# Kernel tuning notes

Hardware: AMD Instinct MI355X
Metric: run time of the kernel (lower is better)

## Reference

```python
import jax, jax.numpy as jnp
import numpy as np

D_MODEL, D_STATE, N_HEADS = 1024, 64, 16


def setup_inputs() -> dict:
    key = jax.random.key(0)
    ks = jax.random.split(key, 4)
    B, T = 4, 4096
    s = 1.0 / np.sqrt(D_MODEL)
    x = jax.random.normal(ks[0], (B, T, D_MODEL), dtype=jnp.float32)
    h_prev = jnp.zeros((B, N_HEADS, D_STATE), dtype=jnp.float32)
    gate_w = jax.random.normal(ks[1], (2 * N_HEADS * D_STATE, D_MODEL), dtype=jnp.float32) * s
    # torch init: forget-gate bias = 1, input-gate bias = 0
    gate_b = jnp.concatenate([jnp.ones(N_HEADS * D_STATE), jnp.zeros(N_HEADS * D_STATE)]).astype(jnp.float32)
    value_w = jax.random.normal(ks[2], (N_HEADS * D_STATE, D_MODEL), dtype=jnp.float32) * s
    out_w = jax.random.normal(ks[3], (D_MODEL, N_HEADS * D_STATE), dtype=jnp.float32) * s
    return {"x": x, "h_prev": h_prev, "gate_w": gate_w, "gate_b": gate_b, "value_w": value_w, "out_w": out_w}


def reference(x, h_prev, gate_w, gate_b, value_w, out_w):
    B, T, _ = x.shape
    H, S = N_HEADS, D_STATE
    gates = (jnp.einsum('btd,gd->btg', x, gate_w) + gate_b).reshape(B, T, 2, H, S)
    A = jax.nn.sigmoid(gates[:, :, 0])   # [B,T,H,S] forget gate
    Bg = jax.nn.sigmoid(gates[:, :, 1])  # [B,T,H,S] input gate
    V = jnp.einsum('btd,vd->btv', x, value_w).reshape(B, T, H, S)

    def step(h, inp):
        a_t, bv_t = inp
        h = a_t * h + bv_t
        return h, h

    # time-major for scan; precompute B*V elementwise product
    a_tm = jnp.moveaxis(A, 1, 0)                # [T,B,H,S]
    bv_tm = jnp.moveaxis(Bg * V, 1, 0)          # [T,B,H,S]
    h_last, h_seq = jax.lax.scan(step, h_prev, (a_tm, bv_tm))
    h_flat = jnp.moveaxis(h_seq, 0, 1).reshape(B, T, H * S)
    y = jnp.einsum('btv,dv->btd', h_flat, out_w)  # dropout is identity at p=0/eval
    return y, h_last
```

## Files before the change

kernel.cpp:

```cpp
#include <hip/hip_runtime.h>
#include <cstdint>
#include <cstddef>


typedef _Float16 f16;
typedef _Float16 f16x2 __attribute__((ext_vector_type(2)));
typedef _Float16 f16x8 __attribute__((ext_vector_type(8)));
typedef float    f32x4 __attribute__((ext_vector_type(4)));

__device__ __forceinline__ void gload_lds16(const void* g, void* l) {
  __builtin_amdgcn_global_load_lds(
      (const __attribute__((address_space(1))) void*)g,
      (__attribute__((address_space(3))) void*)l, 16, 0, 0);
}

__device__ __forceinline__ float sigmoidf_(float x) {
  return 1.0f / (1.0f + __expf(-x));
}

__global__ __launch_bounds__(256) void cast_pack(
    const float* __restrict__ x, const float* __restrict__ gw,
    const float* __restrict__ vw, const float* __restrict__ ow,
    f16* __restrict__ xh, f16* __restrict__ wgv, f16* __restrict__ owb) {
  const int XG = 2097152, GG = 262144, VG = 131072, OG = 131072;
  int id = blockIdx.x * 256 + threadIdx.x;
  const float* src;
  f16* dst;
  if (id < XG) {
    src = x + (size_t)id * 8;
    dst = xh + (size_t)id * 8;
  } else if (id < XG + GG) {
    int g = id - XG;
    int row = g >> 7, col = g & 127;
    int drow = (row < 1024) ? row : (1024 + 2 * (row - 1024));
    src = gw + ((size_t)row << 10) + col * 8;
    dst = wgv + ((size_t)drow << 10) + col * 8;
  } else if (id < XG + GG + VG) {
    int g = id - XG - GG;
    int row = g >> 7, col = g & 127;
    int drow = 1024 + 2 * row + 1;
    src = vw + ((size_t)row << 10) + col * 8;
    dst = wgv + ((size_t)drow << 10) + col * 8;
  } else if (id < XG + GG + VG + OG) {
    int g = id - XG - GG - VG;
    src = ow + (size_t)g * 8;
    dst = owb + (size_t)g * 8;
  } else {
    return;
  }
  float4 v0 = ((const float4*)src)[0], v1 = ((const float4*)src)[1];
  f16x8 o;
  o[0] = (f16)v0.x; o[1] = (f16)v0.y; o[2] = (f16)v0.z; o[3] = (f16)v0.w;
  o[4] = (f16)v1.x; o[5] = (f16)v1.y; o[6] = (f16)v1.z; o[7] = (f16)v1.w;
  *(f16x8*)dst = o;
}

template <int EPI>
__global__ __launch_bounds__(512, 2) void gemm256(
    const f16* __restrict__ A, const f16* __restrict__ Bw,
    const float* __restrict__ gate_b, void* __restrict__ o0v,
    void* __restrict__ o1v, int Mtiles) {
  constexpr int K = 1024;
  __shared__ __align__(16) f16 SH[65536];
  f16* LA = SH;
  f16* LB = SH + 32768;

  const int tid  = threadIdx.x;
  const int lane = tid & 63;
  const int l15  = lane & 15;
  const int oct4 = lane >> 4;
  const int wid  = tid >> 6;
  const int wr   = wid >> 2;
  const int wc   = wid & 3;

  const int nwg = gridDim.x;
  const int bid = blockIdx.x;
  const int swz = (bid & 7) * (nwg >> 3) + (bid >> 3);
  const int m0 = (swz % Mtiles) * 256;
  const int n0 = (swz / Mtiles) * 256;

  const int srow = tid >> 2;
  const int soct = (tid & 3) ^ ((srow >> 1) & 3);
  const f16* Ag = A  + (size_t)(n0 + srow) * K + soct * 8;
  const f16* Bg = Bw + (size_t)(m0 + srow) * K + soct * 8;
  f16* Al = LA + tid * 8;
  f16* Bl = LB + tid * 8;

  const int fswz  = oct4 ^ ((l15 >> 1) & 3);
  const int aslot = (wr * 128 + l15) * 4 + fswz;
  const int bslot = (wc * 64 + l15) * 4 + fswz;

  f32x4 acc[8][4];
#pragma unroll
  for (int mm = 0; mm < 8; ++mm)
#pragma unroll
    for (int nn = 0; nn < 4; ++nn)
#pragma unroll
      for (int e = 0; e < 4; ++e) acc[mm][nn][e] = 0.f;

#define STAGE_A(tl, kh)                                          \
  do {                                                           \
    const f16* s_ = Ag + (tl) * 64 + (kh) * 32;                  \
    f16* d_ = Al + ((tl) & 1) * 16384 + (kh) * 8192;             \
    gload_lds16(s_, d_);                                         \
    gload_lds16(s_ + 128 * K, d_ + 4096);                        \
  } while (0)
#define STAGE_B(tl, kh)                                          \
  do {                                                           \
    const f16* s_ = Bg + (tl) * 64 + (kh) * 32;                  \
    f16* d_ = Bl + ((tl) & 1) * 16384 + (kh) * 8192;             \
    gload_lds16(s_, d_);                                         \
    gload_lds16(s_ + 128 * K, d_ + 4096);                        \
  } while (0)

  STAGE_A(0, 0); STAGE_B(0, 0);
  STAGE_A(0, 1); STAGE_B(0, 1);
  STAGE_A(1, 0); STAGE_B(1, 0);
  asm volatile("s_waitcnt vmcnt(8)" ::: "memory");
  __builtin_amdgcn_s_barrier();
  asm volatile("" ::: "memory");

  f16x8 bf[4];
  for (int i = 0; i < 8; ++i) {
    const bool last = (i == 7);
#pragma unroll
    for (int ph = 0; ph < 8; ++ph) {
      const int bb = ph >> 2;
      const int ks = (ph >> 1) & 1;
      const int h  = ph & 1;

      f16x8 af[4];
      if (h == 0) {
#pragma unroll
        for (int nn = 0; nn < 4; ++nn)
          bf[nn] = *(const f16x8*)&LB[bb * 16384 + ks * 8192 +
                                      (bslot + nn * 64) * 8];
      }
#pragma unroll
      for (int mm = 0; mm < 4; ++mm)
        af[mm] = *(const f16x8*)&LA[bb * 16384 + ks * 8192 +
                                    (aslot + (h * 4 + mm) * 64) * 8];

      {
        constexpr int toff[8] = {1, 1, 2, 2, 2, 2, 3, 3};
        constexpr int khv[8]  = {1, 1, 0, 0, 1, 1, 0, 0};
        if (!last || ph < 2) {
          const int tl = 2 * i + toff[ph];
          if (ph & 1) STAGE_B(tl, khv[ph]); else STAGE_A(tl, khv[ph]);
        }
      }

      __builtin_amdgcn_s_barrier();
      asm volatile("s_waitcnt lgkmcnt(0)" ::: "memory");

      __builtin_amdgcn_s_setprio(1);
#pragma unroll
      for (int mm = 0; mm < 4; ++mm)
#pragma unroll
        for (int nn = 0; nn < 4; ++nn)
          acc[h * 4 + mm][nn] = __builtin_amdgcn_mfma_f32_16x16x32_f16(
              af[mm], bf[nn], acc[h * 4 + mm][nn], 0, 0, 0);
      __builtin_amdgcn_s_setprio(0);

      if (ph & 1) {
        if (!last) {
          asm volatile("s_waitcnt vmcnt(8)" ::: "memory");
        } else if (ph == 1) {
          asm volatile("s_waitcnt vmcnt(8)" ::: "memory");
        } else if (ph == 3) {
          asm volatile("s_waitcnt vmcnt(4)" ::: "memory");
        } else if (ph == 5) {
          asm volatile("s_waitcnt vmcnt(0)" ::: "memory");
        }
      }
      __builtin_amdgcn_s_barrier();
      asm volatile("" ::: "memory");
    }
  }
#undef STAGE_A
#undef STAGE_B

  if (EPI == 1) {
    float* out = (float*)o0v;
#pragma unroll
    for (int mm = 0; mm < 8; ++mm)
#pragma unroll
      for (int nn = 0; nn < 4; ++nn) {
        const int m = m0 + wc * 64 + nn * 16 + l15;
#pragma unroll
        for (int r = 0; r < 4; ++r) {
          const int n = n0 + wr * 128 + mm * 16 + oct4 * 4 + r;
          out[(size_t)n * 1024 + m] = acc[mm][nn][r];
        }
      }
    return;
  }

  if (m0 < 1024) {
    float bias[4];
#pragma unroll
    for (int nn = 0; nn < 4; ++nn)
      bias[nn] = gate_b[m0 + wc * 64 + nn * 16 + l15];
    f16* o0 = (f16*)o0v;
#pragma unroll
    for (int ck = 0; ck < 2; ++ck) {
      __builtin_amdgcn_s_barrier();
      asm volatile("" ::: "memory");
      if (wr == ck) {
#pragma unroll
        for (int mm = 0; mm < 8; ++mm)
#pragma unroll
          for (int nn = 0; nn < 4; ++nn) {
            const int ch = wc * 64 + nn * 16 + l15;
#pragma unroll
            for (int r = 0; r < 4; ++r) {
              const int nl = mm * 16 + oct4 * 4 + r;
              SH[nl * 264 + ch] = (f16)sigmoidf_(acc[mm][nn][r] + bias[nn]);
            }
          }
      }
      __builtin_amdgcn_s_barrier();
      asm volatile("" ::: "memory");
#pragma unroll
      for (int j = 0; j < 8; ++j) {
        int s = j * 512 + tid;
        int row = s >> 5, sl = s & 31;
        f16x8 vv = *(const f16x8*)&SH[row * 264 + sl * 8];
        *(f16x8*)(o0 + (size_t)(n0 + ck * 128 + row) * 1024 + m0 + sl * 8) =
            vv;
      }
    }
  } else {
    const int c0 = (m0 - 1024) >> 1;
    float biasv[4];
#pragma unroll
    for (int nn = 0; nn < 4; ++nn) {
      const int ml = wc * 64 + nn * 16 + l15;
      biasv[nn] = gate_b[1024 + c0 + (ml >> 1)];
    }
    f16* o1 = (f16*)o1v;
#pragma unroll
    for (int ck = 0; ck < 2; ++ck) {
      __builtin_amdgcn_s_barrier();
      asm volatile("" ::: "memory");
      if (wr == ck) {
#pragma unroll
        for (int mm = 0; mm < 8; ++mm)
#pragma unroll
          for (int nn = 0; nn < 4; ++nn) {
            const int ml = wc * 64 + nn * 16 + l15;
#pragma unroll
            for (int r = 0; r < 4; ++r) {
              float val = acc[mm][nn][r];
              float pv = __shfl_xor(val, 1, 64);
              if (!(lane & 1)) {
                const int nl = mm * 16 + oct4 * 4 + r;
                SH[nl * 136 + (ml >> 1)] =
                    (f16)(sigmoidf_(val + biasv[nn]) * pv);
              }
            }
          }
      }
      __builtin_amdgcn_s_barrier();
      asm volatile("" ::: "memory");
#pragma unroll
      for (int j = 0; j < 4; ++j) {
        int s = j * 512 + tid;
        int row = s >> 4, sl = s & 15;
        f16x8 vv = *(const f16x8*)&SH[row * 136 + sl * 8];
        *(f16x8*)(o1 + (size_t)(n0 + ck * 128 + row) * 1024 + c0 + sl * 8) =
            vv;
      }
    }
  }
}

__global__ __launch_bounds__(256) void scan_pass1(
    const f16x2* __restrict__ a, const f16x2* __restrict__ bv,
    float2* __restrict__ Ac, float2* __restrict__ Uc) {
  const int c2 = blockIdx.x * 256 + threadIdx.x;
  const int j = blockIdx.y;
  const int b = blockIdx.z;
  const size_t base = ((size_t)(b * 4096 + j * 32)) * 512 + c2;
  float P0 = 1.f, P1 = 1.f, U0 = 0.f, U1 = 0.f;
#pragma unroll 8
  for (int t = 0; t < 32; ++t) {
    const size_t o = base + (size_t)t * 512;
    f16x2 at = a[o], bt = bv[o];
    float a0 = (float)at[0], a1 = (float)at[1];
    P0 *= a0; P1 *= a1;
    U0 = a0 * U0 + (float)bt[0];
    U1 = a1 * U1 + (float)bt[1];
  }
  const size_t o = ((size_t)(b * 128 + j)) * 512 + c2;
  Ac[o] = make_float2(P0, P1);
  Uc[o] = make_float2(U0, U1);
}

__global__ __launch_bounds__(256) void scan_pass2(
    const float* __restrict__ Ac, const float* __restrict__ Uc,
    const float* __restrict__ h_prev, float* __restrict__ Hs,
    float* __restrict__ hlast) {
  __shared__ float SA[4][64], SU[4][64];
  const int tid = threadIdx.x;
  const int seg = tid >> 6;
  const int cl  = tid & 63;
  const int ch  = blockIdx.x * 64 + cl;
  const int b = ch >> 10, c = ch & 1023;
  float A = 1.f, U = 0.f;
  for (int t = 0; t < 32; ++t) {
    const int j = seg * 32 + t;
    const size_t o = ((size_t)(b * 128 + j)) * 1024 + c;
    float av = Ac[o], uv = Uc[o];
    U = av * U + uv;
    A = av * A;
  }
  SA[seg][cl] = A;
  SU[seg][cl] = U;
  __syncthreads();
  float Ae = 1.f, Ue = 0.f;
  for (int s = 0; s < seg; ++s) {
    float av = SA[s][cl], uv = SU[s][cl];
    Ue = av * Ue + uv;
    Ae = av * Ae;
  }
  float H = Ae * h_prev[b * 1024 + c] + Ue;
  for (int t = 0; t < 32; ++t) {
    const int j = seg * 32 + t;
    const size_t o = ((size_t)(b * 128 + j)) * 1024 + c;
    Hs[o] = H;
    H = Ac[o] * H + Uc[o];
  }
  if (seg == 3) hlast[b * 1024 + c] = H;
}

__global__ __launch_bounds__(256) void scan_pass3(
    const f16x2* __restrict__ a, const f16x2* __restrict__ bv,
    const float2* __restrict__ Hs, f16x2* __restrict__ hb) {
  const int c2 = blockIdx.x * 256 + threadIdx.x;
  const int j = blockIdx.y;
  const int b = blockIdx.z;
  const size_t base = ((size_t)(b * 4096 + j * 32)) * 512 + c2;
  float2 H = Hs[((size_t)(b * 128 + j)) * 512 + c2];
  float h0 = H.x, h1 = H.y;
#pragma unroll 8
  for (int t = 0; t < 32; ++t) {
    const size_t o = base + (size_t)t * 512;
    f16x2 at = a[o], bt = bv[o];
    h0 = (float)at[0] * h0 + (float)bt[0];
    h1 = (float)at[1] * h1 + (float)bt[1];
    f16x2 hv; hv[0] = (f16)h0; hv[1] = (f16)h1;
    hb[o] = hv;
  }
}

extern "C" void kernel_launch(void* const* d_in, const int* in_sizes, int n_in,
                              void* d_out, int out_size, void* d_ws,
                              size_t ws_size, hipStream_t stream) {
  const float* x       = (const float*)d_in[0];
  const float* h_prev  = (const float*)d_in[1];
  const float* gate_w  = (const float*)d_in[2];
  const float* gate_b  = (const float*)d_in[3];
  const float* value_w = (const float*)d_in[4];
  const float* out_w   = (const float*)d_in[5];
  float* out = (float*)d_out;

  char* ws = (char*)d_ws;
  f16*   xh   = (f16*)(ws);
  f16*   wgv  = (f16*)(ws + 33554432);
  f16*   owb  = (f16*)(ws + 39845888);
  f16*   abuf = (f16*)(ws + 41943040);
  f16*   bvb  = (f16*)(ws + 75497472);
  float* Ac   = (float*)(ws + 109051904);
  float* Uc   = (float*)(ws + 111149056);
  float* Hs   = (float*)(ws + 113246208);
  float* hlast = out + 16777216;

  cast_pack<<<10240, 256, 0, stream>>>(x, gate_w, value_w, out_w, xh, wgv,
                                       owb);

  gemm256<0><<<dim3(768), 512, 0, stream>>>(xh, wgv, gate_b, abuf, bvb, 12);

  scan_pass1<<<dim3(2, 128, 4), 256, 0, stream>>>(
      (const f16x2*)abuf, (const f16x2*)bvb, (float2*)Ac, (float2*)Uc);
  scan_pass2<<<64, 256, 0, stream>>>(Ac, Uc, h_prev, Hs, hlast);
  scan_pass3<<<dim3(2, 128, 4), 256, 0, stream>>>(
      (const f16x2*)abuf, (const f16x2*)bvb, (const float2*)Hs, (f16x2*)xh);

  gemm256<1><<<dim3(256), 512, 0, stream>>>(xh, owb, nullptr, out, nullptr, 4);
}
```

Baseline: 377.8 us.

## Restructure GEMM main loop into 4-slot LDS ring with staggered LDS waits

Replaces the 8-phase double-buffered K loop with a fully unrolled loop over 32 k-steps of 32. It uses a 4-slot LDS ring with prefetch distance 2, and a single barrier per k-step instead of two per phase. LDS fragments are read with inline-asm ds_read_b128 using immediate offsets. Waits on lgkmcnt are staggered so MFMAs start once the first fragments land. This aims to cut barrier and wait overhead and overlap LDS reads with MFMA, but full unrolling and holding all fragments raises register pressure and code size.

```diff
diff --git a/kernel.cpp b/kernel.cpp
--- a/kernel.cpp
+++ b/kernel.cpp
@@ -55,6 +55,15 @@
   *(f16x8*)dst = o;
 }
 
+#define DSREAD(dst, addr, off)                                        \
+  asm volatile("ds_read_b128 %0, %1 offset:%2"                       \
+               : "=v"(dst)                                            \
+               : "v"(addr), "i"(off))
+
+#define WAIT_LGKM(n)                                                  \
+  asm volatile("s_waitcnt lgkmcnt(" #n ")" ::: "memory");             \
+  __builtin_amdgcn_sched_barrier(0)
+
 template <int EPI>
 __global__ __launch_bounds__(512, 2) void gemm256(
     const f16* __restrict__ A, const f16* __restrict__ Bw,
@@ -87,8 +96,9 @@
   f16* Bl = LB + tid * 8;
 
   const int fswz  = oct4 ^ ((l15 >> 1) & 3);
-  const int aslot = (wr * 128 + l15) * 4 + fswz;
-  const int bslot = (wc * 64 + l15) * 4 + fswz;
+  const unsigned shbase = (unsigned)(uintptr_t)(&SH[0]);
+  const int aaddr = (int)shbase + ((wr * 128 + l15) * 4 + fswz) * 16;
+  const int baddr = (int)shbase + 65536 + ((wc * 64 + l15) * 4 + fswz) * 16;
 
   f32x4 acc[8][4];
 #pragma unroll
@@ -98,87 +108,70 @@
 #pragma unroll
       for (int e = 0; e < 4; ++e) acc[mm][nn][e] = 0.f;
 
-#define STAGE_A(tl, kh)                                          \
-  do {                                                           \
-    const f16* s_ = Ag + (tl) * 64 + (kh) * 32;                  \
-    f16* d_ = Al + ((tl) & 1) * 16384 + (kh) * 8192;             \
-    gload_lds16(s_, d_);                                         \
-    gload_lds16(s_ + 128 * K, d_ + 4096);                        \
+#define STAGE_AB(kt)                                                  \
+  do {                                                                \
+    const f16* sa_ = Ag + (kt) * 32;                                  \
+    const f16* sb_ = Bg + (kt) * 32;                                  \
+    f16* da_ = Al + ((kt) & 3) * 8192;                                \
+    f16* db_ = Bl + ((kt) & 3) * 8192;                                \
+    gload_lds16(sa_, da_);                                            \
+    gload_lds16(sa_ + 128 * K, da_ + 4096);                           \
+    gload_lds16(sb_, db_);                                            \
+    gload_lds16(sb_ + 128 * K, db_ + 4096);                           \
   } while (0)
-#define STAGE_B(tl, kh)                                          \
-  do {                                                           \
-    const f16* s_ = Bg + (tl) * 64 + (kh) * 32;                  \
-    f16* d_ = Bl + ((tl) & 1) * 16384 + (kh) * 8192;             \
-    gload_lds16(s_, d_);                                         \
-    gload_lds16(s_ + 128 * K, d_ + 4096);                        \
-  } while (0)
-
-  STAGE_A(0, 0); STAGE_B(0, 0);
-  STAGE_A(0, 1); STAGE_B(0, 1);
-  STAGE_A(1, 0); STAGE_B(1, 0);
-  asm volatile("s_waitcnt vmcnt(8)" ::: "memory");
+
+  STAGE_AB(0);
+  STAGE_AB(1);
+  asm volatile("s_waitcnt vmcnt(4)" ::: "memory");
   __builtin_amdgcn_s_barrier();
   asm volatile("" ::: "memory");
 
-  f16x8 bf[4];
-  for (int i = 0; i < 8; ++i) {
-    const bool last = (i == 7);
-#pragma unroll
-    for (int ph = 0; ph < 8; ++ph) {
-      const int bb = ph >> 2;
-      const int ks = (ph >> 1) & 1;
-      const int h  = ph & 1;
-
-      f16x8 af[4];
-      if (h == 0) {
-#pragma unroll
-        for (int nn = 0; nn < 4; ++nn)
-          bf[nn] = *(const f16x8*)&LB[bb * 16384 + ks * 8192 +
-                                      (bslot + nn * 64) * 8];
-      }
-#pragma unroll
-      for (int mm = 0; mm < 4; ++mm)
-        af[mm] = *(const f16x8*)&LA[bb * 16384 + ks * 8192 +
-                                    (aslot + (h * 4 + mm) * 64) * 8];
-
-      {
-        constexpr int toff[8] = {1, 1, 2, 2, 2, 2, 3, 3};
-        constexpr int khv[8]  = {1, 1, 0, 0, 1, 1, 0, 0};
-        if (!last || ph < 2) {
-          const int tl = 2 * i + toff[ph];
-          if (ph & 1) STAGE_B(tl, khv[ph]); else STAGE_A(tl, khv[ph]);
-        }
-      }
-
-      __builtin_amdgcn_s_barrier();
-      asm volatile("s_waitcnt lgkmcnt(0)" ::: "memory");
-
-      __builtin_amdgcn_s_setprio(1);
-#pragma unroll
-      for (int mm = 0; mm < 4; ++mm)
-#pragma unroll
-        for (int nn = 0; nn < 4; ++nn)
-          acc[h * 4 + mm][nn] = __builtin_amdgcn_mfma_f32_16x16x32_f16(
-              af[mm], bf[nn], acc[h * 4 + mm][nn], 0, 0, 0);
-      __builtin_amdgcn_s_setprio(0);
-
-      if (ph & 1) {
-        if (!last) {
-          asm volatile("s_waitcnt vmcnt(8)" ::: "memory");
-        } else if (ph == 1) {
-          asm volatile("s_waitcnt vmcnt(8)" ::: "memory");
-        } else if (ph == 3) {
-          asm volatile("s_waitcnt vmcnt(4)" ::: "memory");
-        } else if (ph == 5) {
-          asm volatile("s_waitcnt vmcnt(0)" ::: "memory");
-        }
-      }
-      __builtin_amdgcn_s_barrier();
-      asm volatile("" ::: "memory");
+#pragma unroll
+  for (int kt = 0; kt < 32; ++kt) {
+    const int roff = (kt & 3) * 16384;
+    const int aP = aaddr + roff;
+    const int bP = baddr + roff;
+    f16x8 af[8], bf[4];
+    DSREAD(bf[0], bP, 0);    DSREAD(bf[1], bP, 1024);
+    DSREAD(bf[2], bP, 2048); DSREAD(bf[3], bP, 3072);
+    DSREAD(af[0], aP, 0);    DSREAD(af[1], aP, 1024);
+    DSREAD(af[2], aP, 2048); DSREAD(af[3], aP, 3072);
+    DSREAD(af[4], aP, 4096); DSREAD(af[5], aP, 5120);
+    DSREAD(af[6], aP, 6144); DSREAD(af[7], aP, 7168);
+
+    if (kt < 30) STAGE_AB(kt + 2);
+
+    __builtin_amdgcn_s_setprio(1);
+    WAIT_LGKM(7);
+#pragma unroll
+    for (int nn = 0; nn < 4; ++nn)
+      acc[0][nn] = __builtin_amdgcn_mfma_f32_16x16x32_f16(
+          af[0], bf[nn], acc[0][nn], 0, 0, 0);
+    WAIT_LGKM(4);
+#pragma unroll
+    for (int mm = 1; mm < 4; ++mm)
+#pragma unroll
+      for (int nn = 0; nn < 4; ++nn)
+        acc[mm][nn] = __builtin_amdgcn_mfma_f32_16x16x32_f16(
+            af[mm], bf[nn], acc[mm][nn], 0, 0, 0);
+    WAIT_LGKM(0);
+#pragma unroll
+    for (int mm = 4; mm < 8; ++mm)
+#pragma unroll
+      for (int nn = 0; nn < 4; ++nn)
+        acc[mm][nn] = __builtin_amdgcn_mfma_f32_16x16x32_f16(
+            af[mm], bf[nn], acc[mm][nn], 0, 0, 0);
+    __builtin_amdgcn_s_setprio(0);
+
+    if (kt < 30) {
+      asm volatile("s_waitcnt vmcnt(4)" ::: "memory");
+    } else if (kt == 30) {
+      asm volatile("s_waitcnt vmcnt(0)" ::: "memory");
     }
-  }
-#undef STAGE_A
-#undef STAGE_B
+    __builtin_amdgcn_s_barrier();
+    asm volatile("" ::: "memory");
+  }
+#undef STAGE_AB
 
   if (EPI == 1) {
     float* out = (float*)o0v;
```

Result: faster. 354.5 us (-6.2%).
